# Optimization experiments

Measured on AMD Instinct MI355X. Metric: run time of the kernel, lower is better.

Reference implementation:

```python
import jax, jax.numpy as jnp
import numpy as np

B, S, HIDDEN = 2, 2048, 1024
NUM_HEADS, HEAD_DIM = 16, 64
STRIDE = 128
NEG = -10000.0


def _strided_mask(seq_len):
    # Sparse Transformer strided pattern: causal, local window of STRIDE,
    # plus every STRIDE-th previous position.
    i = jnp.arange(seq_len)[:, None]
    j = jnp.arange(seq_len)[None, :]
    diff = i - j
    allowed = (diff >= 0) & ((diff < STRIDE) | (diff % STRIDE == 0))
    return jnp.where(allowed, 0.0, NEG).astype(jnp.float32)  # [S, S]


def setup_inputs() -> dict:
    key = jax.random.key(0)
    k0, k1, k2, k3, k4 = jax.random.split(key, 5)
    hidden_states = jax.random.normal(k0, (B, S, HIDDEN), dtype=jnp.float32)
    attention_mask = jnp.zeros((B, 1, 1, S), dtype=jnp.float32)
    W_q = jax.random.normal(k1, (HIDDEN, HIDDEN), dtype=jnp.float32) * 0.02
    b_q = jnp.zeros((HIDDEN,), dtype=jnp.float32)
    W_v = jax.random.normal(k2, (HIDDEN, HIDDEN), dtype=jnp.float32) * 0.02
    b_v = jnp.zeros((HIDDEN,), dtype=jnp.float32)
    return {"hidden_states": hidden_states, "attention_mask": attention_mask,
            "W_q": W_q, "b_q": b_q, "W_v": W_v, "b_v": b_v}


def _heads(x):
    b, s, _ = x.shape
    return x.reshape(b, s, NUM_HEADS, HEAD_DIM).transpose(0, 2, 1, 3)  # [B,H,S,d]


def reference(hidden_states, attention_mask, W_q, b_q, W_v, b_v):
    q = _heads(hidden_states @ W_q + b_q)  # [B,H,S,d]
    v = _heads(hidden_states @ W_v + b_v)  # [B,H,S,d]
    hash_mask = _strided_mask(q.shape[-2])  # [S,S], broadcast over B,H
    # NB: source computes matmul(query, query^T) -- Q used for both sides.
    scores = jnp.einsum('bhid,bhjd->bhij', q, q) + hash_mask
    scores = scores / jnp.sqrt(jnp.asarray(HEAD_DIM, scores.dtype))
    scores = scores + attention_mask
    probs = jax.nn.softmax(scores, axis=-1)  # dropout p=0 (eval)
    ctx = jnp.einsum('bhij,bhjd->bhid', probs, v)  # [B,H,S,d]
    b = ctx.shape[0]
    return ctx.transpose(0, 2, 1, 3).reshape(b, -1, NUM_HEADS * HEAD_DIM)
```

## Files before the change

kernel.cpp:

```cpp
#include <hip/hip_runtime.h>

typedef __attribute__((ext_vector_type(8))) short short8;
typedef __attribute__((ext_vector_type(4))) float float4v;

__device__ inline float bf2f(ushort u) {
    unsigned v = ((unsigned)u) << 16;
    return __builtin_bit_cast(float, v);
}
__device__ inline ushort f2bf(float f) {
    unsigned u = __builtin_bit_cast(unsigned, f);
    u += 0x7FFFu + ((u >> 16) & 1u);
    return (ushort)(u >> 16);
}

__device__ inline void gload_lds16(const ushort* g, ushort* l) {
    __builtin_amdgcn_global_load_lds(
        (const __attribute__((address_space(1))) unsigned int*)g,
        (__attribute__((address_space(3))) unsigned int*)l,
        16, 0, 0);
}

__global__ __launch_bounds__(256) void convert_hs(
    const float* __restrict__ hs, ushort* __restrict__ hsb) {
    const size_t base = ((size_t)blockIdx.x * 256 + threadIdx.x) * 16;
    union { ushort u[16]; uint4 v[2]; } o;
#pragma unroll
    for (int q = 0; q < 4; ++q) {
        float4v f = *(const float4v*)(hs + base + q * 4);
#pragma unroll
        for (int j = 0; j < 4; ++j) o.u[q * 4 + j] = f2bf(f[j]);
    }
    *(uint4*)(hsb + base)     = o.v[0];
    *(uint4*)(hsb + base + 8) = o.v[1];
}

__global__ __launch_bounds__(256) void transpose_w(
    const float* __restrict__ Wq, const float* __restrict__ Wv,
    ushort* __restrict__ Wtq, ushort* __restrict__ Wtv) {
    __shared__ ushort tile[64][68];
    const float* W = blockIdx.z ? Wv : Wq;
    ushort* Wt     = blockIdx.z ? Wtv : Wtq;
    const int k0 = blockIdx.y * 64, n0 = blockIdx.x * 64;
    const int tid = threadIdx.x;
    const int rr = tid >> 4;
    const int cc = (tid & 15) * 4;
    union U4 { ushort u[4]; uint2 v; };
#pragma unroll
    for (int i = 0; i < 4; ++i) {
        int row = rr + i * 16;
        float4v f = *(const float4v*)(W + (size_t)(k0 + row) * 1024 + n0 + cc);
        U4 x;
#pragma unroll
        for (int j = 0; j < 4; ++j) x.u[j] = f2bf(f[j]);
        *(uint2*)&tile[row][cc] = x.v;
    }
    __syncthreads();
#pragma unroll
    for (int i = 0; i < 4; ++i) {
        int row = rr + i * 16;
        U4 o;
#pragma unroll
        for (int j = 0; j < 4; ++j) o.u[j] = tile[cc + j][row];
        *(uint2*)(Wt + (size_t)(n0 + row) * 1024 + k0 + cc) = o.v;
    }
}

__global__ __launch_bounds__(256) void qv_gemm(
    const ushort* __restrict__ hsb,
    const ushort* __restrict__ Wtq, const ushort* __restrict__ Wtv,
    const float* __restrict__ bq, const float* __restrict__ bv,
    ushort* __restrict__ q_ws, ushort* __restrict__ v_ws) {
    __shared__ ushort Al[128 * 64];
    __shared__ ushort Bl[128 * 64];
    const ushort* Wt  = blockIdx.z ? Wtv : Wtq;
    const float* bias = blockIdx.z ? bv : bq;
    ushort* out       = blockIdx.z ? v_ws : q_ws;
    const int m0 = blockIdx.y * 128, n0 = blockIdx.x * 128;
    const int tid = threadIdx.x;
    const int wid = tid >> 6, lane = tid & 63;
    const int quad = lane >> 4, l16 = lane & 15;
    const int wm = (wid >> 1) * 64, wn = (wid & 1) * 64;
    const int rbase = 32 * wid;
    const int srow = lane >> 3, scol = (lane & 7) * 8;

    float4v acc[4][4] = {};

    for (int kt = 0; kt < 1024; kt += 64) {
        __syncthreads();
#pragma unroll
        for (int c8 = 0; c8 < 4; ++c8) {
            int row = rbase + c8 * 8;
            gload_lds16(hsb + (size_t)(m0 + row + srow) * 1024 + kt + scol,
                        &Al[row * 64]);
            gload_lds16(Wt + (size_t)(n0 + row + srow) * 1024 + kt + scol,
                        &Bl[row * 64]);
        }
        __syncthreads();
#pragma unroll
        for (int ks = 0; ks < 2; ++ks) {
            short8 af[4], bfr[4];
#pragma unroll
            for (int mt = 0; mt < 4; ++mt)
                af[mt] = *(const short8*)&Al[(wm + mt * 16 + l16) * 64 + (ks * 4 + quad) * 8];
#pragma unroll
            for (int nt = 0; nt < 4; ++nt)
                bfr[nt] = *(const short8*)&Bl[(wn + nt * 16 + l16) * 64 + (ks * 4 + quad) * 8];
#pragma unroll
            for (int mt = 0; mt < 4; ++mt)
#pragma unroll
                for (int nt = 0; nt < 4; ++nt)
                    acc[mt][nt] = __builtin_amdgcn_mfma_f32_16x16x32_bf16(
                        af[mt], bfr[nt], acc[mt][nt], 0, 0, 0);
        }
    }
#pragma unroll
    for (int mt = 0; mt < 4; ++mt) {
#pragma unroll
        for (int nt = 0; nt < 4; ++nt) {
            int coln = n0 + wn + nt * 16 + l16;
            float bsv = bias[coln];
            int hh = coln >> 6, dd = coln & 63;
#pragma unroll
            for (int reg = 0; reg < 4; ++reg) {
                int r = m0 + wm + mt * 16 + quad * 4 + reg;
                int bb = r >> 11, s = r & 2047;
                out[(((size_t)bb * 16 + hh) * 2048 + s) * 64 + dd] =
                    f2bf(acc[mt][nt][reg] + bsv);
            }
        }
    }
}

__global__ __launch_bounds__(512) void attn(
    const ushort* __restrict__ q_ws, const ushort* __restrict__ v_ws,
    const float* __restrict__ amask, float* __restrict__ out) {
    const int lin = blockIdx.x + 16 * blockIdx.y;
    const int u8 = lin & 7, v32 = lin >> 3;
    const int t = v32 & 15;
    const int h = u8 + ((v32 >> 4) << 3);
    const int b = blockIdx.z;

    __shared__ ushort Kw[256][72];
    __shared__ ushort Vt[64][266];
    __shared__ ushort Pl[128][266];
    __shared__ float  Sstr[128][17];
    __shared__ float  am[2048];

    const int tid = threadIdx.x;
    const int wid = tid >> 6, lane = tid & 63;
    const int quad = lane >> 4, l16 = lane & 15;
    const int r0 = wid * 16;
    const size_t qbase = ((size_t)b * 16 + h) * 2048 * 64;
    const int base_row = (t - 1) * 128;
    const int nk = (t >= 2) ? (t - 1) : 0;

    *(float4v*)&am[tid * 4] = *(const float4v*)(amask + (size_t)b * 2048 + tid * 4);
#pragma unroll
    for (int i = 0; i < 4; ++i) {
        int c = tid + i * 512;
        int row = c >> 3, col = (c & 7) * 8;
        int jg = base_row + row; if (jg < 0) jg = 0;
        *(uint4*)&Kw[row][col] = *(const uint4*)(q_ws + qbase + (size_t)jg * 64 + col);
    }
    {
        int j = tid & 255, dh0 = (tid >> 8) * 32;
        int jg = base_row + j; if (jg < 0) jg = 0;
        const ushort* src = v_ws + qbase + (size_t)jg * 64 + dh0;
#pragma unroll
        for (int d = 0; d < 32; d += 8) {
            union { uint4 v; ushort u[8]; } tmp;
            tmp.v = *(const uint4*)(src + d);
#pragma unroll
            for (int jj = 0; jj < 8; ++jj) Vt[dh0 + d + jj][j] = tmp.u[jj];
        }
    }
    __syncthreads();

    float4v sacc[16] = {};
#pragma unroll
    for (int ks = 0; ks < 2; ++ks) {
        short8 af = *(const short8*)&Kw[128 + r0 + l16][ks * 32 + quad * 8];
#pragma unroll
        for (int nt = 0; nt < 16; ++nt) {
            short8 bfr = *(const short8*)&Kw[nt * 16 + l16][ks * 32 + quad * 8];
            sacc[nt] = __builtin_amdgcn_mfma_f32_16x16x32_bf16(af, bfr, sacc[nt], 0, 0, 0);
        }
    }

    const int sr = tid >> 2;
    const int dq = (tid & 3) * 16;
    if (nk > 0) {
        float qv[16];
#pragma unroll
        for (int d = 0; d < 16; d += 8) {
            union { uint4 v; ushort u[8]; } tmp;
            tmp.v = *(const uint4*)&Kw[128 + sr][dq + d];
#pragma unroll
            for (int j = 0; j < 8; ++j) qv[d + j] = bf2f(tmp.u[j]);
        }
        for (int k = 0; k < nk; ++k) {
            const ushort* kr = q_ws + qbase + (size_t)(k * 128 + sr) * 64 + dq;
            float p = 0.f;
#pragma unroll
            for (int d = 0; d < 16; d += 8) {
                union { uint4 v; ushort u[8]; } tmp;
                tmp.v = *(const uint4*)(kr + d);
#pragma unroll
                for (int jj = 0; jj < 8; ++jj) p += qv[d + jj] * bf2f(tmp.u[jj]);
            }
            p += __shfl_xor(p, 1);
            p += __shfl_xor(p, 2);
            if ((tid & 3) == 0)
                Sstr[sr][k] = p * 0.125f + am[k * 128 + sr];
        }
    }
    __syncthreads();

#pragma unroll
    for (int reg = 0; reg < 4; ++reg) {
        int rr = r0 + quad * 4 + reg;
        float sv[16];
#pragma unroll
        for (int nt = 0; nt < 16; ++nt) {
            int c = nt * 16 + l16;
            bool allowed = (c >= rr) && (c <= rr + 128) && (t > 0 || c >= 128);
            int ci = base_row + c; if (ci < 0) ci = 0;
            sv[nt] = allowed ? sacc[nt][reg] * 0.125f + am[ci] : -INFINITY;
        }
        float sstr_v = (l16 < nk) ? Sstr[rr][l16] : -INFINITY;
        float m = sstr_v;
#pragma unroll
        for (int nt = 0; nt < 16; ++nt) m = fmaxf(m, sv[nt]);
#pragma unroll
        for (int off = 1; off < 16; off <<= 1) m = fmaxf(m, __shfl_xor(m, off));

        float es = (l16 < nk) ? __expf(sstr_v - m) : 0.f;
        float sum = es;
#pragma unroll
        for (int nt = 0; nt < 16; ++nt) {
            float e = (sv[nt] == -INFINITY) ? 0.f : __expf(sv[nt] - m);
            sv[nt] = e; sum += e;
        }
#pragma unroll
        for (int off = 1; off < 16; off <<= 1) sum += __shfl_xor(sum, off);
        float rden = 1.f / sum;
#pragma unroll
        for (int nt = 0; nt < 16; ++nt)
            Pl[rr][nt * 16 + l16] = f2bf(sv[nt] * rden);
        if (l16 < nk)
            Sstr[rr][l16] = es * rden;
    }
    __syncthreads();

    float4v cacc[4] = {};
#pragma unroll
    for (int ks = 0; ks < 8; ++ks) {
        short8 af = *(const short8*)&Pl[r0 + l16][ks * 32 + quad * 8];
#pragma unroll
        for (int nt = 0; nt < 4; ++nt) {
            short8 bfr = *(const short8*)&Vt[nt * 16 + l16][ks * 32 + quad * 8];
            cacc[nt] = __builtin_amdgcn_mfma_f32_16x16x32_bf16(af, bfr, cacc[nt], 0, 0, 0);
        }
    }
    __syncthreads();

    float* ctxp = (float*)&Pl[0][0];
    {
        float acc16[16] = {};
        for (int k = 0; k < nk; ++k) {
            float p = Sstr[sr][k];
            const ushort* vr = v_ws + qbase + (size_t)(k * 128 + sr) * 64 + dq;
#pragma unroll
            for (int d = 0; d < 16; d += 8) {
                union { uint4 v; ushort u[8]; } tmp;
                tmp.v = *(const uint4*)(vr + d);
#pragma unroll
                for (int j = 0; j < 8; ++j) acc16[d + j] += p * bf2f(tmp.u[j]);
            }
        }
#pragma unroll
        for (int d = 0; d < 16; d += 4)
            *(float4v*)&ctxp[sr * 68 + dq + d] = *(const float4v*)&acc16[d];
    }
    __syncthreads();

    const size_t obase = ((size_t)b * 2048 + (size_t)t * 128) * 1024 + (size_t)h * 64;
#pragma unroll
    for (int nt = 0; nt < 4; ++nt)
#pragma unroll
        for (int reg = 0; reg < 4; ++reg) {
            int rr = r0 + quad * 4 + reg;
            int d = nt * 16 + l16;
            out[obase + (size_t)rr * 1024 + d] = cacc[nt][reg] + ctxp[rr * 68 + d];
        }
}

extern "C" void kernel_launch(void* const* d_in, const int* in_sizes, int n_in,
                              void* d_out, int out_size, void* d_ws, size_t ws_size,
                              hipStream_t stream) {
    int ihs = -1, iam = -1, iw1 = -1, iw2 = -1, ib1 = -1, ib2 = -1;
    for (int i = 0; i < n_in; ++i) {
        int s = in_sizes[i];
        if      (s == 4194304) { if (ihs < 0) ihs = i; }
        else if (s == 4096)    { if (iam < 0) iam = i; }
        else if (s == 1048576) { if (iw1 < 0) iw1 = i; else if (iw2 < 0) iw2 = i; }
        else if (s == 1024)    { if (ib1 < 0) ib1 = i; else if (ib2 < 0) ib2 = i; }
    }
    if (ihs < 0) ihs = 0; if (iam < 0) iam = 1;
    if (iw1 < 0) iw1 = 2; if (ib1 < 0) ib1 = 3;
    if (iw2 < 0) iw2 = 4; if (ib2 < 0) ib2 = 5;

    const float* hs    = (const float*)d_in[ihs];
    const float* amask = (const float*)d_in[iam];
    const float* Wq    = (const float*)d_in[iw1];
    const float* bq    = (const float*)d_in[ib1];
    const float* Wv    = (const float*)d_in[iw2];
    const float* bv    = (const float*)d_in[ib2];
    float* out = (float*)d_out;

    char* ws = (char*)d_ws;
    ushort* Wtq  = (ushort*)(ws);
    ushort* Wtv  = (ushort*)(ws + (1u << 21));
    ushort* hsb  = (ushort*)(ws + (2u << 21));
    ushort* q_ws = (ushort*)(ws + (2u << 21) + (1u << 23));
    ushort* v_ws = (ushort*)(ws + (2u << 21) + (2u << 23));

    convert_hs<<<1024, 256, 0, stream>>>(hs, hsb);
    transpose_w<<<dim3(16, 16, 2), 256, 0, stream>>>(Wq, Wv, Wtq, Wtv);
    qv_gemm<<<dim3(8, 32, 2), 256, 0, stream>>>(hsb, Wtq, Wtv, bq, bv, q_ws, v_ws);
    attn<<<dim3(16, 16, 2), 512, 0, stream>>>(q_ws, v_ws, amask, out);
}
```

Measured before the change: 152.1 us.

## Shrink attention LDS footprint with XOR-swizzled shared buffers and split P·V

Replaces the padded K, V-transposed and P shared arrays with two 32KB XOR-swizzled buffers. The probability tile reuses the K buffer by running P·V in two halves, with the second half's probabilities held in packed registers. It also shrinks the mask cache to a 256-entry window, reads the strided mask straight from global memory, and requests 4 blocks per CU in launch bounds. The aim is to cut LDS use and bank conflicts so more blocks fit per CU, at the cost of an extra barrier and store pass plus more register pressure.

```diff
diff --git a/kernel.cpp b/kernel.cpp
--- a/kernel.cpp
+++ b/kernel.cpp
@@ -131,20 +131,15 @@
     }
 }
 
-__global__ __launch_bounds__(512) void attn(
+__global__ __launch_bounds__(512, 4) void attn(
     const ushort* __restrict__ q_ws, const ushort* __restrict__ v_ws,
     const float* __restrict__ amask, float* __restrict__ out) {
-    const int lin = blockIdx.x + 16 * blockIdx.y;
-    const int u8 = lin & 7, v32 = lin >> 3;
-    const int t = v32 & 15;
-    const int h = u8 + ((v32 >> 4) << 3);
-    const int b = blockIdx.z;
-
-    __shared__ ushort Kw[256][72];
-    __shared__ ushort Vt[64][266];
-    __shared__ ushort Pl[128][266];
+    const int t = blockIdx.x, h = blockIdx.y, b = blockIdx.z;
+
+    __shared__ ushort KwPl[16384];
+    __shared__ ushort VtS[16384];
     __shared__ float  Sstr[128][17];
-    __shared__ float  am[2048];
+    __shared__ float  amw[256];
 
     const int tid = threadIdx.x;
     const int wid = tid >> 6, lane = tid & 63;
@@ -154,24 +149,32 @@
     const int base_row = (t - 1) * 128;
     const int nk = (t >= 2) ? (t - 1) : 0;
 
-    *(float4v*)&am[tid * 4] = *(const float4v*)(amask + (size_t)b * 2048 + tid * 4);
+    if (tid < 256) {
+        int j = base_row + tid; if (j < 0) j = 0;
+        amw[tid] = amask[(size_t)b * 2048 + j];
+    }
 #pragma unroll
     for (int i = 0; i < 4; ++i) {
-        int c = tid + i * 512;
-        int row = c >> 3, col = (c & 7) * 8;
+        int u = tid + i * 512;
+        int row = u >> 3, c = u & 7;
         int jg = base_row + row; if (jg < 0) jg = 0;
-        *(uint4*)&Kw[row][col] = *(const uint4*)(q_ws + qbase + (size_t)jg * 64 + col);
+        *(uint4*)&KwPl[row * 64 + ((c ^ (row & 7)) * 8)] =
+            *(const uint4*)(q_ws + qbase + (size_t)jg * 64 + c * 8);
     }
     {
         int j = tid & 255, dh0 = (tid >> 8) * 32;
         int jg = base_row + j; if (jg < 0) jg = 0;
         const ushort* src = v_ws + qbase + (size_t)jg * 64 + dh0;
+        int cj = j >> 3, j7 = j & 7;
 #pragma unroll
         for (int d = 0; d < 32; d += 8) {
             union { uint4 v; ushort u[8]; } tmp;
             tmp.v = *(const uint4*)(src + d);
 #pragma unroll
-            for (int jj = 0; jj < 8; ++jj) Vt[dh0 + d + jj][j] = tmp.u[jj];
+            for (int jj = 0; jj < 8; ++jj) {
+                int dd = dh0 + d + jj;
+                VtS[dd * 256 + ((cj ^ (dd & 7)) * 8) + j7] = tmp.u[jj];
+            }
         }
     }
     __syncthreads();
@@ -179,10 +182,12 @@
     float4v sacc[16] = {};
 #pragma unroll
     for (int ks = 0; ks < 2; ++ks) {
-        short8 af = *(const short8*)&Kw[128 + r0 + l16][ks * 32 + quad * 8];
+        int c = ks * 4 + quad;
+        int sw = (c ^ (l16 & 7)) * 8;
+        short8 af = *(const short8*)&KwPl[(128 + r0 + l16) * 64 + sw];
 #pragma unroll
         for (int nt = 0; nt < 16; ++nt) {
-            short8 bfr = *(const short8*)&Kw[nt * 16 + l16][ks * 32 + quad * 8];
+            short8 bfr = *(const short8*)&KwPl[(nt * 16 + l16) * 64 + sw];
             sacc[nt] = __builtin_amdgcn_mfma_f32_16x16x32_bf16(af, bfr, sacc[nt], 0, 0, 0);
         }
     }
@@ -192,30 +197,32 @@
     if (nk > 0) {
         float qv[16];
 #pragma unroll
-        for (int d = 0; d < 16; d += 8) {
-            union { uint4 v; ushort u[8]; } tmp;
-            tmp.v = *(const uint4*)&Kw[128 + sr][dq + d];
-#pragma unroll
-            for (int j = 0; j < 8; ++j) qv[d + j] = bf2f(tmp.u[j]);
+        for (int cc = 0; cc < 2; ++cc) {
+            int c = (dq >> 3) + cc;
+            union { uint4 v; ushort u[8]; } tm;
+            tm.v = *(const uint4*)&KwPl[(128 + sr) * 64 + ((c ^ (sr & 7)) * 8)];
+#pragma unroll
+            for (int jj = 0; jj < 8; ++jj) qv[cc * 8 + jj] = bf2f(tm.u[jj]);
         }
         for (int k = 0; k < nk; ++k) {
-            const ushort* kr = q_ws + qbase + (size_t)(k * 128 + sr) * 64 + dq;
+            const ushort* kr = q_ws + qbase + (size_t)(sr + (k << 7)) * 64 + dq;
             float p = 0.f;
 #pragma unroll
             for (int d = 0; d < 16; d += 8) {
-                union { uint4 v; ushort u[8]; } tmp;
-                tmp.v = *(const uint4*)(kr + d);
-#pragma unroll
-                for (int jj = 0; jj < 8; ++jj) p += qv[d + jj] * bf2f(tmp.u[jj]);
+                union { uint4 v; ushort u[8]; } tm;
+                tm.v = *(const uint4*)(kr + d);
+#pragma unroll
+                for (int jj = 0; jj < 8; ++jj) p += qv[d + jj] * bf2f(tm.u[jj]);
             }
             p += __shfl_xor(p, 1);
             p += __shfl_xor(p, 2);
             if ((tid & 3) == 0)
-                Sstr[sr][k] = p * 0.125f + am[k * 128 + sr];
-        }
-    }
-    __syncthreads();
-
+                Sstr[sr][k] = p * 0.125f + amask[(size_t)b * 2048 + sr + (k << 7)];
+        }
+    }
+    __syncthreads();
+
+    unsigned pb[4][4];
 #pragma unroll
     for (int reg = 0; reg < 4; ++reg) {
         int rr = r0 + quad * 4 + reg;
@@ -224,8 +231,7 @@
         for (int nt = 0; nt < 16; ++nt) {
             int c = nt * 16 + l16;
             bool allowed = (c >= rr) && (c <= rr + 128) && (t > 0 || c >= 128);
-            int ci = base_row + c; if (ci < 0) ci = 0;
-            sv[nt] = allowed ? sacc[nt][reg] * 0.125f + am[ci] : -INFINITY;
+            sv[nt] = allowed ? sacc[nt][reg] * 0.125f + amw[c] : -INFINITY;
         }
         float sstr_v = (l16 < nk) ? Sstr[rr][l16] : -INFINITY;
         float m = sstr_v;
@@ -245,42 +251,85 @@
         for (int off = 1; off < 16; off <<= 1) sum += __shfl_xor(sum, off);
         float rden = 1.f / sum;
 #pragma unroll
-        for (int nt = 0; nt < 16; ++nt)
-            Pl[rr][nt * 16 + l16] = f2bf(sv[nt] * rden);
-        if (l16 < nk)
-            Sstr[rr][l16] = es * rden;
+        for (int nt = 0; nt < 8; ++nt) {
+            int c = nt * 2 + (l16 >> 3);
+            KwPl[rr * 128 + ((c ^ (rr & 15)) * 8) + (l16 & 7)] = f2bf(sv[nt] * rden);
+        }
+#pragma unroll
+        for (int i2 = 0; i2 < 4; ++i2) {
+            unsigned lo = f2bf(sv[8 + 2 * i2] * rden);
+            unsigned hi = f2bf(sv[9 + 2 * i2] * rden);
+            pb[reg][i2] = lo | (hi << 16);
+        }
+        if (l16 < nk) Sstr[rr][l16] = es * rden;
     }
     __syncthreads();
 
     float4v cacc[4] = {};
 #pragma unroll
-    for (int ks = 0; ks < 8; ++ks) {
-        short8 af = *(const short8*)&Pl[r0 + l16][ks * 32 + quad * 8];
+    for (int ks = 0; ks < 4; ++ks) {
+        int cp = ks * 4 + quad;
+        short8 af = *(const short8*)&KwPl[(r0 + l16) * 128 + ((cp ^ l16) * 8)];
 #pragma unroll
         for (int nt = 0; nt < 4; ++nt) {
-            short8 bfr = *(const short8*)&Vt[nt * 16 + l16][ks * 32 + quad * 8];
+            int sw = (cp ^ (l16 & 7)) * 8;
+            short8 bfr = *(const short8*)&VtS[(nt * 16 + l16) * 256 + sw];
             cacc[nt] = __builtin_amdgcn_mfma_f32_16x16x32_bf16(af, bfr, cacc[nt], 0, 0, 0);
         }
     }
     __syncthreads();
 
-    float* ctxp = (float*)&Pl[0][0];
+#pragma unroll
+    for (int reg = 0; reg < 4; ++reg) {
+        int rr = r0 + quad * 4 + reg;
+#pragma unroll
+        for (int i2 = 0; i2 < 4; ++i2) {
+            int nt0 = 8 + 2 * i2;
+#pragma unroll
+            for (int e2 = 0; e2 < 2; ++e2) {
+                int nt = nt0 + e2;
+                int c = (nt - 8) * 2 + (l16 >> 3);
+                ushort val = (ushort)((pb[reg][i2] >> (16 * e2)) & 0xFFFF);
+                KwPl[rr * 128 + ((c ^ (rr & 15)) * 8) + (l16 & 7)] = val;
+            }
+        }
+    }
+    __syncthreads();
+
+#pragma unroll
+    for (int ks = 0; ks < 4; ++ks) {
+        int cp = ks * 4 + quad;
+        short8 af = *(const short8*)&KwPl[(r0 + l16) * 128 + ((cp ^ l16) * 8)];
+#pragma unroll
+        for (int nt = 0; nt < 4; ++nt) {
+            int cv = 16 + cp;
+            int sw = (cv ^ (l16 & 7)) * 8;
+            short8 bfr = *(const short8*)&VtS[(nt * 16 + l16) * 256 + sw];
+            cacc[nt] = __builtin_amdgcn_mfma_f32_16x16x32_bf16(af, bfr, cacc[nt], 0, 0, 0);
+        }
+    }
+    __syncthreads();
+
+    float* ctxp = (float*)&VtS[0];
     {
         float acc16[16] = {};
         for (int k = 0; k < nk; ++k) {
             float p = Sstr[sr][k];
-            const ushort* vr = v_ws + qbase + (size_t)(k * 128 + sr) * 64 + dq;
+            const ushort* vr = v_ws + qbase + (size_t)(sr + (k << 7)) * 64 + dq;
 #pragma unroll
             for (int d = 0; d < 16; d += 8) {
-                union { uint4 v; ushort u[8]; } tmp;
-                tmp.v = *(const uint4*)(vr + d);
-#pragma unroll
-                for (int j = 0; j < 8; ++j) acc16[d + j] += p * bf2f(tmp.u[j]);
-            }
-        }
-#pragma unroll
-        for (int d = 0; d < 16; d += 4)
-            *(float4v*)&ctxp[sr * 68 + dq + d] = *(const float4v*)&acc16[d];
+                union { uint4 v; ushort u[8]; } tm;
+                tm.v = *(const uint4*)(vr + d);
+#pragma unroll
+                for (int jj = 0; jj < 8; ++jj) acc16[d + jj] += p * bf2f(tm.u[jj]);
+            }
+        }
+#pragma unroll
+        for (int d4 = 0; d4 < 4; ++d4) {
+            int c = (dq >> 2) + d4;
+            *(float4v*)&ctxp[sr * 64 + ((c ^ (sr & 15)) * 4)] =
+                *(const float4v*)&acc16[d4 * 4];
+        }
     }
     __syncthreads();
 
@@ -291,7 +340,8 @@
         for (int reg = 0; reg < 4; ++reg) {
             int rr = r0 + quad * 4 + reg;
             int d = nt * 16 + l16;
-            out[obase + (size_t)rr * 1024 + d] = cacc[nt][reg] + ctxp[rr * 68 + d];
+            float cstr = ctxp[rr * 64 + (((d >> 2) ^ (rr & 15)) * 4) + (d & 3)];
+            out[obase + (size_t)rr * 1024 + d] = cacc[nt][reg] + cstr;
         }
 }
 
```

After: 149.7 us. About the same (-1.6%).
